# Performance work log

Measured on AMD Instinct MI355X. Metric: run time of the kernel, lower is better.

Reference implementation:

```python
import jax, jax.numpy as jnp
import numpy as np


def setup_inputs() -> dict:
    key = jax.random.key(0)
    ks = jax.random.split(key, 7)
    B, H, W, C = 8, 64, 64, 8
    d = C // 8  # q/k/v channels (= 1 here; forced by the module's broadcast-add)
    x = jax.random.normal(ks[0], (B, H, W, C), dtype=jnp.float32)
    # 1x1 convs == per-pixel linear layers: weight (C, d), bias (d,)
    scale = 1.0 / np.sqrt(C)
    Wq = jax.random.normal(ks[1], (C, d), dtype=jnp.float32) * scale
    bq = jnp.zeros((d,), dtype=jnp.float32)
    Wk = jax.random.normal(ks[2], (C, d), dtype=jnp.float32) * scale
    bk = jnp.zeros((d,), dtype=jnp.float32)
    Wv = jax.random.normal(ks[3], (C, d), dtype=jnp.float32) * scale
    bv = jnp.zeros((d,), dtype=jnp.float32)
    gamma = jnp.float32(0.5)  # nonzero so the attention branch matters
    return {"x": x, "Wq": Wq, "bq": bq, "Wk": Wk, "bk": bk, "Wv": Wv, "bv": bv, "gamma": gamma}


def reference(x, Wq, bq, Wk, bk, Wv, bv, gamma):
    B, H, W, C = x.shape
    N = H * W
    # 1x1 conv projections (NHWC, per-pixel linear)
    q = (jnp.einsum('bhwc,cd->bhwd', x, Wq) + bq).reshape(B, N, -1)  # (B,N,d)
    k = (jnp.einsum('bhwc,cd->bhwd', x, Wk) + bk).reshape(B, N, -1)  # (B,N,d)
    v = (jnp.einsum('bhwc,cd->bhwd', x, Wv) + bv).reshape(B, N, -1)  # (B,N,d)
    # energy[b,i,j] = <q_i, k_j>; NOTE: no 1/sqrt(d) scaling, per source
    energy = jnp.einsum('bnd,bmd->bnm', q, k)  # (B,N,N)
    attention = jax.nn.softmax(energy, axis=-1)
    # out[b,i,d] = sum_j attention[b,i,j] * v[b,j,d]
    out = jnp.einsum('bnm,bmd->bnd', attention, v).reshape(B, H, W, -1)  # (B,H,W,d)
    # gamma-scaled residual; d==1 so out broadcasts against C channels
    y = out * gamma + x
    return (y, attention)
```

## Files before the change

### kernel.cpp

```cpp
#include <hip/hip_runtime.h>
#include <math.h>

#define NPIX 4096
#define CCH 8
#define ROWS 32
#define BLK 256
#define NW   (BLK/64)
#define NP   (BLK/ROWS)
#define SEG  (NPIX/NP)
#define L2E 1.44269504088896340736f

typedef float floatx4 __attribute__((ext_vector_type(4)));

__global__ __launch_bounds__(BLK) void attn_fused(
    const float* __restrict__ x,
    const float* __restrict__ Wq, const float* __restrict__ bq,
    const float* __restrict__ Wk, const float* __restrict__ bk,
    const float* __restrict__ Wv, const float* __restrict__ bv,
    const float* __restrict__ gamma_p,
    float* __restrict__ y, float* __restrict__ attn)
{
    __shared__ float ks[NPIX];
    __shared__ float vs[NPIX];
    __shared__ float qrow[ROWS];
    __shared__ float crow[ROWS];
    __shared__ float spart[NP][ROWS];
    __shared__ float opart[NP][ROWS];
    __shared__ float kred[2][NW];

    const int b = blockIdx.y;
    const int rowbase = blockIdx.x * ROWS;
    const int tid = threadIdx.x;
    const int wid = tid >> 6;
    const int lane = tid & 63;

    float wq[CCH], wk[CCH], wv[CCH];
#pragma unroll
    for (int c = 0; c < CCH; ++c) { wq[c] = Wq[c]; wk[c] = Wk[c]; wv[c] = Wv[c]; }
    const float bqv = bq[0], bkv = bk[0], bvv = bv[0];
    const float gamma = gamma_p[0];

    const float* xb = x + (size_t)b * NPIX * CCH;

    float kmx = -INFINITY, kmn = INFINITY;
    for (int j = tid; j < NPIX; j += BLK) {
        const float4* xp = reinterpret_cast<const float4*>(xb + (size_t)j * CCH);
        float4 x0 = xp[0];
        float4 x1 = xp[1];
        float kj = bkv;
        kj = fmaf(x0.x, wk[0], kj); kj = fmaf(x0.y, wk[1], kj);
        kj = fmaf(x0.z, wk[2], kj); kj = fmaf(x0.w, wk[3], kj);
        kj = fmaf(x1.x, wk[4], kj); kj = fmaf(x1.y, wk[5], kj);
        kj = fmaf(x1.z, wk[6], kj); kj = fmaf(x1.w, wk[7], kj);
        float vj = bvv;
        vj = fmaf(x0.x, wv[0], vj); vj = fmaf(x0.y, wv[1], vj);
        vj = fmaf(x0.z, wv[2], vj); vj = fmaf(x0.w, wv[3], vj);
        vj = fmaf(x1.x, wv[4], vj); vj = fmaf(x1.y, wv[5], vj);
        vj = fmaf(x1.z, wv[6], vj); vj = fmaf(x1.w, wv[7], vj);
        ks[j] = kj;
        vs[j] = vj;
        kmx = fmaxf(kmx, kj);
        kmn = fminf(kmn, kj);
    }
#pragma unroll
    for (int off = 32; off > 0; off >>= 1) {
        kmx = fmaxf(kmx, __shfl_xor(kmx, off));
        kmn = fminf(kmn, __shfl_xor(kmn, off));
    }
    if (lane == 0) { kred[0][wid] = kmx; kred[1][wid] = kmn; }
    __syncthreads();
    kmx = fmaxf(fmaxf(kred[0][0], kred[0][1]), fmaxf(kred[0][2], kred[0][3]));
    kmn = fminf(fminf(kred[1][0], kred[1][1]), fminf(kred[1][2], kred[1][3]));

    const int r = tid & (ROWS - 1);
    const int p = tid >> 5;
    const int i = rowbase + r;
    const float4* xq = reinterpret_cast<const float4*>(xb + (size_t)i * CCH);
    float4 a0 = xq[0];
    float4 a1 = xq[1];
    float q = bqv;
    q = fmaf(a0.x, wq[0], q); q = fmaf(a0.y, wq[1], q);
    q = fmaf(a0.z, wq[2], q); q = fmaf(a0.w, wq[3], q);
    q = fmaf(a1.x, wq[4], q); q = fmaf(a1.y, wq[5], q);
    q = fmaf(a1.z, wq[6], q); q = fmaf(a1.w, wq[7], q);

    const float q2 = q * L2E;
    const float m2 = q2 * ((q >= 0.f) ? kmx : kmn);

    float s0 = 0.f, s1 = 0.f, s2 = 0.f, s3 = 0.f;
    float o0 = 0.f, o1 = 0.f, o2 = 0.f, o3 = 0.f;
    const int j0 = p * SEG;
    for (int j = j0; j < j0 + SEG; j += 4) {
        float4 kk = *reinterpret_cast<const float4*>(&ks[j]);
        float4 vv = *reinterpret_cast<const float4*>(&vs[j]);
        float e0 = exp2f(fmaf(q2, kk.x, -m2));
        float e1 = exp2f(fmaf(q2, kk.y, -m2));
        float e2 = exp2f(fmaf(q2, kk.z, -m2));
        float e3 = exp2f(fmaf(q2, kk.w, -m2));
        s0 += e0; s1 += e1; s2 += e2; s3 += e3;
        o0 = fmaf(e0, vv.x, o0);
        o1 = fmaf(e1, vv.y, o1);
        o2 = fmaf(e2, vv.z, o2);
        o3 = fmaf(e3, vv.w, o3);
    }
    spart[p][r] = (s0 + s1) + (s2 + s3);
    opart[p][r] = (o0 + o1) + (o2 + o3);
    __syncthreads();

    if (tid < ROWS) {
        float s = 0.f, o = 0.f;
#pragma unroll
        for (int pp = 0; pp < NP; ++pp) { s += spart[pp][tid]; o += opart[pp][tid]; }
        const float outv = o / s;
        const float og = outv * gamma;
        const int i2 = rowbase + tid;
        const float4* xr = reinterpret_cast<const float4*>(xb + (size_t)i2 * CCH);
        float4 b0 = xr[0];
        float4 b1 = xr[1];
        float* yp = y + ((size_t)b * NPIX + i2) * CCH;
        float4 y0 = { og + b0.x, og + b0.y, og + b0.z, og + b0.w };
        float4 y1 = { og + b1.x, og + b1.y, og + b1.z, og + b1.w };
        *reinterpret_cast<float4*>(yp) = y0;
        *reinterpret_cast<float4*>(yp + 4) = y1;
        qrow[tid] = q2;
        crow[tid] = m2 + log2f(s);
    }
    __syncthreads();

    const int j4 = tid * 4;
    float4 kk0 = *reinterpret_cast<const float4*>(&ks[j4]);
    float4 kk1 = *reinterpret_cast<const float4*>(&ks[j4 + BLK * 4]);
    float4 kk2 = *reinterpret_cast<const float4*>(&ks[j4 + BLK * 8]);
    float4 kk3 = *reinterpret_cast<const float4*>(&ks[j4 + BLK * 12]);

    float* ap0 = attn + ((size_t)b * NPIX + rowbase) * (size_t)NPIX;
    for (int rr = 0; rr < ROWS; ++rr) {
        const float qr = qrow[rr];
        const float cr = crow[rr];
        float* ap = ap0 + (size_t)rr * NPIX;
        floatx4 e0, e1, e2, e3;
        e0.x = exp2f(fmaf(qr, kk0.x, -cr)); e0.y = exp2f(fmaf(qr, kk0.y, -cr));
        e0.z = exp2f(fmaf(qr, kk0.z, -cr)); e0.w = exp2f(fmaf(qr, kk0.w, -cr));
        e1.x = exp2f(fmaf(qr, kk1.x, -cr)); e1.y = exp2f(fmaf(qr, kk1.y, -cr));
        e1.z = exp2f(fmaf(qr, kk1.z, -cr)); e1.w = exp2f(fmaf(qr, kk1.w, -cr));
        e2.x = exp2f(fmaf(qr, kk2.x, -cr)); e2.y = exp2f(fmaf(qr, kk2.y, -cr));
        e2.z = exp2f(fmaf(qr, kk2.z, -cr)); e2.w = exp2f(fmaf(qr, kk2.w, -cr));
        e3.x = exp2f(fmaf(qr, kk3.x, -cr)); e3.y = exp2f(fmaf(qr, kk3.y, -cr));
        e3.z = exp2f(fmaf(qr, kk3.z, -cr)); e3.w = exp2f(fmaf(qr, kk3.w, -cr));
        __builtin_nontemporal_store(e0, reinterpret_cast<floatx4*>(&ap[j4]));
        __builtin_nontemporal_store(e1, reinterpret_cast<floatx4*>(&ap[j4 + BLK * 4]));
        __builtin_nontemporal_store(e2, reinterpret_cast<floatx4*>(&ap[j4 + BLK * 8]));
        __builtin_nontemporal_store(e3, reinterpret_cast<floatx4*>(&ap[j4 + BLK * 12]));
    }
}

extern "C" void kernel_launch(void* const* d_in, const int* in_sizes, int n_in,
                              void* d_out, int out_size, void* d_ws, size_t ws_size,
                              hipStream_t stream) {
    const float* x   = (const float*)d_in[0];
    const float* Wq  = (const float*)d_in[1];
    const float* bq  = (const float*)d_in[2];
    const float* Wk  = (const float*)d_in[3];
    const float* bk  = (const float*)d_in[4];
    const float* Wv  = (const float*)d_in[5];
    const float* bv  = (const float*)d_in[6];
    const float* gm  = (const float*)d_in[7];

    const int B = in_sizes[0] / (NPIX * CCH);
    float* y    = (float*)d_out;
    float* attn = y + (size_t)B * NPIX * CCH;

    dim3 grid(NPIX / ROWS, B);
    attn_fused<<<grid, BLK, 0, stream>>>(x, Wq, bq, Wk, bk, Wv, bv, gm, y, attn);
}
```

Baseline: 122.1 us.

## Split fused attention into stats kernel and separate attention-matrix write kernel

Splits the single kernel into two. The first computes the softmax statistics and y, and saves per-row (q, log-normaliser) pairs to workspace. The second recomputes k in registers and writes the attention matrix with 16 rows per block, so there are more, lighter blocks that need no shared memory for the write-bound phase. The aim is better occupancy and store throughput for the dominant write of the attention matrix, at the cost of an extra launch and recomputing k. The fused kernel stays as a fallback when workspace is too small, and it now contains an odd redundant rewrite of the e3 computation.

```diff
diff --git a/kernel.cpp b/kernel.cpp
--- a/kernel.cpp
+++ b/kernel.cpp
@@ -8,22 +8,21 @@
 #define NW   (BLK/64)
 #define NP   (BLK/ROWS)
 #define SEG  (NPIX/NP)
+#define RB   16
 #define L2E 1.44269504088896340736f
 
 typedef float floatx4 __attribute__((ext_vector_type(4)));
 
-__global__ __launch_bounds__(BLK) void attn_fused(
+__global__ __launch_bounds__(BLK) void attn_stats(
     const float* __restrict__ x,
     const float* __restrict__ Wq, const float* __restrict__ bq,
     const float* __restrict__ Wk, const float* __restrict__ bk,
     const float* __restrict__ Wv, const float* __restrict__ bv,
     const float* __restrict__ gamma_p,
-    float* __restrict__ y, float* __restrict__ attn)
+    float* __restrict__ y, float2* __restrict__ qc)
 {
     __shared__ float ks[NPIX];
     __shared__ float vs[NPIX];
-    __shared__ float qrow[ROWS];
-    __shared__ float crow[ROWS];
     __shared__ float spart[NP][ROWS];
     __shared__ float opart[NP][ROWS];
     __shared__ float kred[2][NW];
@@ -122,6 +121,177 @@
         float4 y1 = { og + b1.x, og + b1.y, og + b1.z, og + b1.w };
         *reinterpret_cast<float4*>(yp) = y0;
         *reinterpret_cast<float4*>(yp + 4) = y1;
+        float2 t;
+        t.x = q2;
+        t.y = m2 + log2f(s);
+        qc[(size_t)b * NPIX + i2] = t;
+    }
+}
+
+__global__ __launch_bounds__(BLK) void attn_write(
+    const float* __restrict__ x,
+    const float* __restrict__ Wk, const float* __restrict__ bk,
+    const float2* __restrict__ qc,
+    float* __restrict__ attn)
+{
+    const int b = blockIdx.y;
+    const int rowbase = blockIdx.x * RB;
+    const int tid = threadIdx.x;
+
+    float wk[CCH];
+#pragma unroll
+    for (int c = 0; c < CCH; ++c) wk[c] = Wk[c];
+    const float bkv = bk[0];
+
+    const float* xb = x + (size_t)b * NPIX * CCH;
+
+    float4 kc[4];
+#pragma unroll
+    for (int g = 0; g < 4; ++g) {
+        const int jg = tid * 4 + g * (BLK * 4);
+        float ke[4];
+#pragma unroll
+        for (int e = 0; e < 4; ++e) {
+            const float4* xp = reinterpret_cast<const float4*>(xb + (size_t)(jg + e) * CCH);
+            float4 x0 = xp[0];
+            float4 x1 = xp[1];
+            float kj = bkv;
+            kj = fmaf(x0.x, wk[0], kj); kj = fmaf(x0.y, wk[1], kj);
+            kj = fmaf(x0.z, wk[2], kj); kj = fmaf(x0.w, wk[3], kj);
+            kj = fmaf(x1.x, wk[4], kj); kj = fmaf(x1.y, wk[5], kj);
+            kj = fmaf(x1.z, wk[6], kj); kj = fmaf(x1.w, wk[7], kj);
+            ke[e] = kj;
+        }
+        kc[g].x = ke[0]; kc[g].y = ke[1]; kc[g].z = ke[2]; kc[g].w = ke[3];
+    }
+
+    const float2* qcb = qc + (size_t)b * NPIX + rowbase;
+    float* ap0 = attn + ((size_t)b * NPIX + rowbase) * (size_t)NPIX + tid * 4;
+
+#pragma unroll 2
+    for (int rr = 0; rr < RB; ++rr) {
+        const float2 t = qcb[rr];
+        const float qr = t.x;
+        const float cr = t.y;
+        float* ap = ap0 + (size_t)rr * NPIX;
+#pragma unroll
+        for (int g = 0; g < 4; ++g) {
+            floatx4 e;
+            e.x = exp2f(fmaf(qr, kc[g].x, -cr));
+            e.y = exp2f(fmaf(qr, kc[g].y, -cr));
+            e.z = exp2f(fmaf(qr, kc[g].z, -cr));
+            e.w = exp2f(fmaf(qr, kc[g].w, -cr));
+            __builtin_nontemporal_store(e, reinterpret_cast<floatx4*>(ap + g * (BLK * 4)));
+        }
+    }
+}
+
+__global__ __launch_bounds__(BLK) void attn_fused(
+    const float* __restrict__ x,
+    const float* __restrict__ Wq, const float* __restrict__ bq,
+    const float* __restrict__ Wk, const float* __restrict__ bk,
+    const float* __restrict__ Wv, const float* __restrict__ bv,
+    const float* __restrict__ gamma_p,
+    float* __restrict__ y, float* __restrict__ attn)
+{
+    __shared__ float ks[NPIX];
+    __shared__ float vs[NPIX];
+    __shared__ float qrow[ROWS];
+    __shared__ float crow[ROWS];
+    __shared__ float spart[NP][ROWS];
+    __shared__ float opart[NP][ROWS];
+    __shared__ float kred[2][NW];
+
+    const int b = blockIdx.y;
+    const int rowbase = blockIdx.x * ROWS;
+    const int tid = threadIdx.x;
+    const int wid = tid >> 6;
+    const int lane = tid & 63;
+
+    float wq[CCH], wk[CCH], wv[CCH];
+#pragma unroll
+    for (int c = 0; c < CCH; ++c) { wq[c] = Wq[c]; wk[c] = Wk[c]; wv[c] = Wv[c]; }
+    const float bqv = bq[0], bkv = bk[0], bvv = bv[0];
+    const float gamma = gamma_p[0];
+    const float* xb = x + (size_t)b * NPIX * CCH;
+
+    float kmx = -INFINITY, kmn = INFINITY;
+    for (int j = tid; j < NPIX; j += BLK) {
+        const float4* xp = reinterpret_cast<const float4*>(xb + (size_t)j * CCH);
+        float4 x0 = xp[0];
+        float4 x1 = xp[1];
+        float kj = bkv;
+        kj = fmaf(x0.x, wk[0], kj); kj = fmaf(x0.y, wk[1], kj);
+        kj = fmaf(x0.z, wk[2], kj); kj = fmaf(x0.w, wk[3], kj);
+        kj = fmaf(x1.x, wk[4], kj); kj = fmaf(x1.y, wk[5], kj);
+        kj = fmaf(x1.z, wk[6], kj); kj = fmaf(x1.w, wk[7], kj);
+        float vj = bvv;
+        vj = fmaf(x0.x, wv[0], vj); vj = fmaf(x0.y, wv[1], vj);
+        vj = fmaf(x0.z, wv[2], vj); vj = fmaf(x0.w, wv[3], vj);
+        vj = fmaf(x1.x, wv[4], vj); vj = fmaf(x1.y, wv[5], vj);
+        vj = fmaf(x1.z, wv[6], vj); vj = fmaf(x1.w, wv[7], vj);
+        ks[j] = kj; vs[j] = vj;
+        kmx = fmaxf(kmx, kj); kmn = fminf(kmn, kj);
+    }
+#pragma unroll
+    for (int off = 32; off > 0; off >>= 1) {
+        kmx = fmaxf(kmx, __shfl_xor(kmx, off));
+        kmn = fminf(kmn, __shfl_xor(kmn, off));
+    }
+    if (lane == 0) { kred[0][wid] = kmx; kred[1][wid] = kmn; }
+    __syncthreads();
+    kmx = fmaxf(fmaxf(kred[0][0], kred[0][1]), fmaxf(kred[0][2], kred[0][3]));
+    kmn = fminf(fminf(kred[1][0], kred[1][1]), fminf(kred[1][2], kred[1][3]));
+
+    const int r = tid & (ROWS - 1);
+    const int p = tid >> 5;
+    const int i = rowbase + r;
+    const float4* xq = reinterpret_cast<const float4*>(xb + (size_t)i * CCH);
+    float4 a0 = xq[0];
+    float4 a1 = xq[1];
+    float q = bqv;
+    q = fmaf(a0.x, wq[0], q); q = fmaf(a0.y, wq[1], q);
+    q = fmaf(a0.z, wq[2], q); q = fmaf(a0.w, wq[3], q);
+    q = fmaf(a1.x, wq[4], q); q = fmaf(a1.y, wq[5], q);
+    q = fmaf(a1.z, wq[6], q); q = fmaf(a1.w, wq[7], q);
+    const float q2 = q * L2E;
+    const float m2 = q2 * ((q >= 0.f) ? kmx : kmn);
+
+    float s0 = 0.f, s1 = 0.f, s2 = 0.f, s3 = 0.f;
+    float o0 = 0.f, o1 = 0.f, o2 = 0.f, o3 = 0.f;
+    const int j0 = p * SEG;
+    for (int j = j0; j < j0 + SEG; j += 4) {
+        float4 kk = *reinterpret_cast<const float4*>(&ks[j]);
+        float4 vv = *reinterpret_cast<const float4*>(&vs[j]);
+        float e0 = exp2f(fmaf(q2, kk.x, -m2));
+        float e1 = exp2f(fmaf(q2, kk.y, -m2));
+        float e2 = exp2f(fmaf(q2, kk.z, -m2));
+        float e3 = exp2f(fmaf(q2, kk.w, -m2));
+        s0 += e0; s1 += e1; s2 += e2; s3 += e3;
+        o0 = fmaf(e0, vv.x, o0);
+        o1 = fmaf(e1, vv.y, o1);
+        o2 = fmaf(e2, vv.z, o2);
+        o3 = fmaf(e3, vv.w, o3);
+    }
+    spart[p][r] = (s0 + s1) + (s2 + s3);
+    opart[p][r] = (o0 + o1) + (o2 + o3);
+    __syncthreads();
+
+    if (tid < ROWS) {
+        float s = 0.f, o = 0.f;
+#pragma unroll
+        for (int pp = 0; pp < NP; ++pp) { s += spart[pp][tid]; o += opart[pp][tid]; }
+        const float outv = o / s;
+        const float og = outv * gamma;
+        const int i2 = rowbase + tid;
+        const float4* xr = reinterpret_cast<const float4*>(xb + (size_t)i2 * CCH);
+        float4 b0 = xr[0];
+        float4 b1 = xr[1];
+        float* yp = y + ((size_t)b * NPIX + i2) * CCH;
+        float4 y0 = { og + b0.x, og + b0.y, og + b0.z, og + b0.w };
+        float4 y1 = { og + b1.x, og + b1.y, og + b1.z, og + b1.w };
+        *reinterpret_cast<float4*>(yp) = y0;
+        *reinterpret_cast<float4*>(yp + 4) = y1;
         qrow[tid] = q2;
         crow[tid] = m2 + log2f(s);
     }
@@ -146,7 +316,9 @@
         e2.x = exp2f(fmaf(qr, kk2.x, -cr)); e2.y = exp2f(fmaf(qr, kk2.y, -cr));
         e2.z = exp2f(fmaf(qr, kk2.z, -cr)); e2.w = exp2f(fmaf(qr, kk2.w, -cr));
         e3.x = exp2f(fmaf(qr, kk3.x, -cr)); e3.y = exp2f(fmaf(qr, kk3.y, -cr));
-        e3.z = exp2f(fmaf(qr, kk3.z, -cr)); e3.w = exp2f(fmaf(qr, kk3.w, -cr));
+        e3.z = exp2f(fmaf(qr, kk3.w == kk3.w ? kk3.w : kk3.w, -cr));
+        e3.w = exp2f(fmaf(qr, kk3.w, -cr));
+        e3.z = exp2f(fmaf(qr, kk3.z, -cr));
         __builtin_nontemporal_store(e0, reinterpret_cast<floatx4*>(&ap[j4]));
         __builtin_nontemporal_store(e1, reinterpret_cast<floatx4*>(&ap[j4 + BLK * 4]));
         __builtin_nontemporal_store(e2, reinterpret_cast<floatx4*>(&ap[j4 + BLK * 8]));
@@ -170,6 +342,15 @@
     float* y    = (float*)d_out;
     float* attn = y + (size_t)B * NPIX * CCH;
 
-    dim3 grid(NPIX / ROWS, B);
-    attn_fused<<<grid, BLK, 0, stream>>>(x, Wq, bq, Wk, bk, Wv, bv, gm, y, attn);
+    const size_t qc_bytes = (size_t)B * NPIX * sizeof(float2);
+    if (ws_size >= qc_bytes) {
+        float2* qc = (float2*)d_ws;
+        dim3 gridA(NPIX / ROWS, B);
+        attn_stats<<<gridA, BLK, 0, stream>>>(x, Wq, bq, Wk, bk, Wv, bv, gm, y, qc);
+        dim3 gridB(NPIX / RB, B);
+        attn_write<<<gridB, BLK, 0, stream>>>(x, Wk, bk, qc, attn);
+    } else {
+        dim3 grid(NPIX / ROWS, B);
+        attn_fused<<<grid, BLK, 0, stream>>>(x, Wq, bq, Wk, bk, Wv, bv, gm, y, attn);
+    }
 }
```

New measurement: 146.7 us. 1.2x slower.
